# Kernel tuning notes

Hardware: AMD Instinct MI355X
Metric: run time of the kernel (lower is better)

Reference implementation:

```python
import math
import jax, jax.numpy as jnp
import numpy as np

B, T, D = 4, 2048, 1024
H, DH = 16, 64
FF = 4096
EPS = 1e-5


def setup_inputs() -> dict:
    key = jax.random.key(0)
    ks = jax.random.split(key, 12)
    s = 0.02
    inp = {
        "x": jax.random.normal(ks[0], (B, T, D), dtype=jnp.float32),
        "ln1_g": jnp.ones((D,), jnp.float32),
        "ln1_b": jnp.zeros((D,), jnp.float32),
        "ln2_g": jnp.ones((D,), jnp.float32),
        "ln2_b": jnp.zeros((D,), jnp.float32),
        # torch nn.Linear convention: weight shape [out, in], y = x @ W.T + b
        "wq": jax.random.normal(ks[1], (D, D), jnp.float32) * s,
        "bq": jnp.zeros((D,), jnp.float32),
        "wk": jax.random.normal(ks[2], (D, D), jnp.float32) * s,
        "bk": jnp.zeros((D,), jnp.float32),
        "wv": jax.random.normal(ks[3], (D, D), jnp.float32) * s,
        "bv": jnp.zeros((D,), jnp.float32),
        "wo": jax.random.normal(ks[4], (D, D), jnp.float32) * s,
        "bo": jnp.zeros((D,), jnp.float32),
        "w1": jax.random.normal(ks[5], (FF, D), jnp.float32) * s,
        "b1": jnp.zeros((FF,), jnp.float32),
        "w2": jax.random.normal(ks[6], (D, FF), jnp.float32) * s,
        "b2": jnp.zeros((D,), jnp.float32),
    }
    return inp


def _layernorm(h, g, b):
    mu = jnp.mean(h, axis=-1, keepdims=True)
    var = jnp.mean(jnp.square(h - mu), axis=-1, keepdims=True)
    return (h - mu) * jax.lax.rsqrt(var + EPS) * g + b


def _block(x, ln1_g, ln1_b, ln2_g, ln2_b, wq, bq, wk, bk, wv, bv, wo, bo, w1, b1, w2, b2):
    b, t, d = x.shape
    h = _layernorm(x, ln1_g, ln1_b)
    q = (h @ wq.T + bq).reshape(b, t, H, DH)
    k = (h @ wk.T + bk).reshape(b, t, H, DH)
    v = (h @ wv.T + bv).reshape(b, t, H, DH)
    # full (non-causal) attention, as in the torch module
    att = jnp.einsum("bqhd,bkhd->bhqk", q, k) / math.sqrt(DH)
    att = jax.nn.softmax(att, axis=-1)
    out = jnp.einsum("bhqk,bkhd->bqhd", att, v).reshape(b, t, d)
    x = x + (out @ wo.T + bo)
    h2 = _layernorm(x, ln2_g, ln2_b)
    ff = jax.nn.gelu(h2 @ w1.T + b1, approximate=False) @ w2.T + b2
    return x + ff


def reference(x, ln1_g, ln1_b, ln2_g, ln2_b, wq, bq, wk, bk, wv, bv, wo, bo, w1, b1, w2, b2):
    return _block(x, ln1_g, ln1_b, ln2_g, ln2_b, wq, bq, wk, bk, wv, bv, wo, bo, w1, b1, w2, b2)
```

## Files before the change

kernel.cpp:

```cpp
#include <hip/hip_runtime.h>
#include <cstdint>
#include <cstddef>

typedef __attribute__((ext_vector_type(8))) __bf16 bf16x8;
typedef __attribute__((ext_vector_type(4))) float f32x4;
typedef __attribute__((ext_vector_type(8))) unsigned short us8;
typedef __attribute__((ext_vector_type(4))) unsigned short us4;

__device__ inline unsigned short f2bf(float f) {
    unsigned int u = __float_as_uint(f);
    u += 0x7fffu + ((u >> 16) & 1u);
    return (unsigned short)(u >> 16);
}

__device__ inline unsigned int pkbf_t(float hi, float lo) {
    return __builtin_amdgcn_perm(__float_as_uint(hi), __float_as_uint(lo), 0x07060302u);
}

__device__ inline void async_copy16(const void* g, void* l) {
    __builtin_amdgcn_global_load_lds(
        (const __attribute__((address_space(1))) unsigned int*)g,
        (__attribute__((address_space(3))) unsigned int*)l, 16, 0, 0);
}

__global__ __launch_bounds__(256) void cvt_bf16(const float* __restrict__ in,
                                                unsigned short* __restrict__ out, int n4) {
    int i = blockIdx.x * 256 + threadIdx.x;
    if (i < n4) {
        float4 v = ((const float4*)in)[i];
        us4 o;
        o[0] = f2bf(v.x); o[1] = f2bf(v.y); o[2] = f2bf(v.z); o[3] = f2bf(v.w);
        ((us4*)out)[i] = o;
    }
}

__global__ __launch_bounds__(256) void ln_bf16(const float* __restrict__ X,
                                               const float* __restrict__ g,
                                               const float* __restrict__ b,
                                               unsigned short* __restrict__ out) {
    int row = blockIdx.x;
    int t = threadIdx.x;
    float4 v = ((const float4*)(X + (size_t)row * 1024))[t];
    float s  = v.x + v.y + v.z + v.w;
    float s2 = v.x * v.x + v.y * v.y + v.z * v.z + v.w * v.w;
#pragma unroll
    for (int m = 1; m < 64; m <<= 1) {
        s  += __shfl_xor(s, m, 64);
        s2 += __shfl_xor(s2, m, 64);
    }
    __shared__ float red[8];
    int w = t >> 6, l = t & 63;
    if (l == 0) { red[w] = s; red[4 + w] = s2; }
    __syncthreads();
    s  = red[0] + red[1] + red[2] + red[3];
    s2 = red[4] + red[5] + red[6] + red[7];
    float mu  = s * (1.0f / 1024.0f);
    float var = s2 * (1.0f / 1024.0f) - mu * mu;
    float rs  = rsqrtf(var + 1e-5f);
    int c = t * 4;
    float4 gv = *(const float4*)(g + c);
    float4 bv = *(const float4*)(b + c);
    us4 o;
    o[0] = f2bf((v.x - mu) * rs * gv.x + bv.x);
    o[1] = f2bf((v.y - mu) * rs * gv.y + bv.y);
    o[2] = f2bf((v.z - mu) * rs * gv.z + bv.z);
    o[3] = f2bf((v.w - mu) * rs * gv.w + bv.w);
    *(us4*)(out + (size_t)row * 1024 + c) = o;
}

#define BM 256
#define BN 256
#define BK 64

template <int EPI>
__global__ __launch_bounds__(512, 2) void gemm_nt(const unsigned short* __restrict__ A,
                                                  const unsigned short* __restrict__ B,
                                                  const float* __restrict__ bias,
                                                  const float* __restrict__ resid,
                                                  void* __restrict__ Cout, int N, int K) {
    __shared__ __align__(16) unsigned short As[2][BM * BK];
    __shared__ __align__(16) unsigned short Bs[2][BN * BK];
    const int tid = threadIdx.x;
    const int lane = tid & 63, w = tid >> 6;
    const int quad = lane >> 4, l16 = lane & 15;
    const int wr = w >> 2, wc = w & 3;
    const int sw = l16 & 7;

    const int gx = gridDim.x;
    const int nwg = gx * gridDim.y;
    int wg = blockIdx.y * gx + blockIdx.x;
    if (!(nwg & 7)) wg = (wg & 7) * (nwg >> 3) + (wg >> 3);
    const size_t bm = (size_t)(wg / gx) * BM;
    const size_t bn = (size_t)(wg % gx) * BN;

    const unsigned short* pA[4];
    const unsigned short* pB[4];
#pragma unroll
    for (int j = 0; j < 4; j++) {
        int c = j * 512 + tid;
        int row = c >> 3;
        int sc = (c & 7) ^ (row & 7);
        pA[j] = A + (bm + row) * (size_t)K + sc * 8;
        pB[j] = B + (bn + row) * (size_t)K + sc * 8;
    }

#define STAGE(buf, kt)                                                        \
    {                                                                         \
        const int koff = (kt)*BK;                                             \
        _Pragma("unroll") for (int j = 0; j < 4; j++)                         \
            async_copy16(pA[j] + koff, &As[buf][(j * 512 + tid) * 8]);        \
        _Pragma("unroll") for (int j = 0; j < 4; j++)                         \
            async_copy16(pB[j] + koff, &Bs[buf][(j * 512 + tid) * 8]);        \
    }

    f32x4 acc[8][4];
#pragma unroll
    for (int i = 0; i < 8; i++)
#pragma unroll
        for (int j = 0; j < 4; j++) acc[i][j] = (f32x4){0.f, 0.f, 0.f, 0.f};

    const int nk = K / BK;

    STAGE(0, 0);
    STAGE(1, 1);
    asm volatile("s_waitcnt vmcnt(8)" ::: "memory");
    __builtin_amdgcn_sched_barrier(0);
    asm volatile("s_barrier" ::: "memory");

    for (int kt = 0; kt < nk; ++kt) {
        const int r = kt & 1;
        const unsigned short* Asr = As[r];
        const unsigned short* Bsr = Bs[r];
#pragma unroll
        for (int kc = 0; kc < 2; kc++) {
            bf16x8 bfr[4];
#pragma unroll
            for (int nf = 0; nf < 4; nf++) {
                int row = wc * 64 + nf * 16 + l16;
                bfr[nf] = *(const bf16x8*)&Bsr[row * 64 + (((kc * 4 + quad) ^ sw) << 3)];
            }
#pragma unroll
            for (int mh = 0; mh < 2; mh++) {
                bf16x8 af[4];
#pragma unroll
                for (int i = 0; i < 4; i++) {
                    int row = wr * 128 + (mh * 4 + i) * 16 + l16;
                    af[i] = *(const bf16x8*)&Asr[row * 64 + (((kc * 4 + quad) ^ sw) << 3)];
                }
                __builtin_amdgcn_s_setprio(1);
#pragma unroll
                for (int i = 0; i < 4; i++)
#pragma unroll
                    for (int nf = 0; nf < 4; nf++)
                        acc[mh * 4 + i][nf] = __builtin_amdgcn_mfma_f32_16x16x32_bf16(
                            af[i], bfr[nf], acc[mh * 4 + i][nf], 0, 0, 0);
                __builtin_amdgcn_s_setprio(0);
                asm volatile("s_barrier" ::: "memory");
            }
        }
        if (kt + 2 < nk) {
            STAGE(r, kt + 2);
            asm volatile("s_waitcnt vmcnt(8)" ::: "memory");
            __builtin_amdgcn_sched_barrier(0);
            asm volatile("s_barrier" ::: "memory");
        } else if (kt + 1 < nk) {
            asm volatile("s_waitcnt vmcnt(0)" ::: "memory");
            __builtin_amdgcn_sched_barrier(0);
            asm volatile("s_barrier" ::: "memory");
        }
    }
#undef STAGE

#pragma unroll
    for (int mf = 0; mf < 8; mf++) {
#pragma unroll
        for (int nf = 0; nf < 4; nf++) {
#pragma unroll
            for (int rr = 0; rr < 4; rr++) {
                size_t row = bm + wr * 128 + mf * 16 + quad * 4 + rr;
                size_t col = bn + wc * 64 + nf * 16 + l16;
                float v = acc[mf][nf][rr] + bias[col];
                if (EPI == 1) {
                    v = 0.5f * v * (1.0f + erff(v * 0.70710678118654752f));
                    ((unsigned short*)Cout)[row * N + col] = f2bf(v);
                } else if (EPI == 2) {
                    ((float*)Cout)[row * N + col] = v + resid[row * N + col];
                } else if (EPI == 6) {
                    int sel = (int)(bn >> 10);
                    if (sel == 0) {
                        ((unsigned short*)Cout)[row * 1024 + col] =
                            f2bf(v * 0.18033688011112042f);
                    } else {
                        int key = (int)row & 2047;
                        int bh  = (((int)row >> 11) << 4) | (((int)col >> 6) & 15);
                        int dh  = (int)col & 63;
                        size_t addr;
                        if (sel == 1)
                            addr = 8388608 + (size_t)bh * 131072 +
                                   (size_t)(key >> 6) * 4096 + (size_t)(key & 63) * 64 +
                                   ((((dh >> 3) ^ (key & 7))) << 3) + (dh & 7);
                        else
                            addr = 16777216 + (size_t)bh * 131072 +
                                   (size_t)(key >> 6) * 4096 + (size_t)dh * 64 +
                                   (((((key >> 3) & 7) ^ (dh & 7))) << 3) + (key & 7);
                        ((unsigned short*)Cout)[addr] = f2bf(v);
                    }
                }
            }
        }
    }
}

__global__ __launch_bounds__(256) void attn_kernel(const unsigned short* __restrict__ Q,
                                                   const unsigned short* __restrict__ Kb,
                                                   const unsigned short* __restrict__ Vtb,
                                                   unsigned short* __restrict__ O) {
    const int bh   = blockIdx.x >> 4;
    const int qblk = blockIdx.x & 15;
    const int b = bh >> 4, h = bh & 15;
    const int tid = threadIdx.x, lane = tid & 63, w = tid >> 6;
    const int quad = lane >> 4, l16 = lane & 15;
    const int sw = l16 & 7;

    __shared__ __align__(16) unsigned short smem[20480];
    unsigned short* Vts = smem + 8192;
    unsigned short* Psw = smem + 12288 + w * 2048;

    const size_t qrow0 = (size_t)b * 2048 + (size_t)qblk * 128 + w * 32;
    const int hcol = h * 64;

    bf16x8 qfr[2][2];
#pragma unroll
    for (int qf = 0; qf < 2; qf++)
#pragma unroll
        for (int kp = 0; kp < 2; kp++)
            qfr[qf][kp] = *(const bf16x8*)(Q + (qrow0 + qf * 16 + l16) * 1024 +
                                           hcol + kp * 32 + quad * 8);

    const unsigned short* ksrc = Kb  + (size_t)bh * 131072;
    const unsigned short* vsrc = Vtb + (size_t)bh * 131072;

    async_copy16(ksrc + tid * 8,        smem + tid * 8);
    async_copy16(ksrc + 2048 + tid * 8, smem + 2048 + tid * 8);
    async_copy16(vsrc + tid * 8,        Vts + tid * 8);
    async_copy16(vsrc + 2048 + tid * 8, Vts + 2048 + tid * 8);

    f32x4 acc[4][2];
#pragma unroll
    for (int df = 0; df < 4; df++)
#pragma unroll
        for (int qf = 0; qf < 2; qf++) acc[df][qf] = (f32x4){0.f, 0.f, 0.f, 0.f};
    float l_[2] = {0.f, 0.f};

    for (int kt = 0; kt < 32; ++kt) {
        unsigned short* Ks = (kt & 1) ? (smem + 4096) : smem;
        if (kt < 31) {
            unsigned short* Kd = (kt & 1) ? smem : (smem + 4096);
            const unsigned short* kg = ksrc + (size_t)(kt + 1) * 4096;
            async_copy16(kg + tid * 8,        Kd + tid * 8);
            async_copy16(kg + 2048 + tid * 8, Kd + 2048 + tid * 8);
            asm volatile("s_waitcnt vmcnt(4)" ::: "memory");
        } else {
            asm volatile("s_waitcnt vmcnt(2)" ::: "memory");
        }
        asm volatile("s_barrier" ::: "memory");

        f32x4 s[4][2];
#pragma unroll
        for (int mf = 0; mf < 4; mf++)
#pragma unroll
            for (int qf = 0; qf < 2; qf++) s[mf][qf] = (f32x4){0.f, 0.f, 0.f, 0.f};
        __builtin_amdgcn_s_setprio(1);
#pragma unroll
        for (int kp = 0; kp < 2; kp++) {
#pragma unroll
            for (int mf = 0; mf < 4; mf++) {
                bf16x8 kf = *(const bf16x8*)&Ks[(mf * 16 + l16) * 64 +
                                                (((kp * 4 + quad) ^ sw) << 3)];
#pragma unroll
                for (int qf = 0; qf < 2; qf++)
                    s[mf][qf] = __builtin_amdgcn_mfma_f32_16x16x32_bf16(kf, qfr[qf][kp],
                                                                        s[mf][qf], 0, 0, 0);
            }
        }
        __builtin_amdgcn_s_setprio(0);

#pragma unroll
        for (int mf = 0; mf < 4; mf++)
#pragma unroll
            for (int qf = 0; qf < 2; qf++) {
                float e0 = exp2f(s[mf][qf][0]);
                float e1 = exp2f(s[mf][qf][1]);
                float e2 = exp2f(s[mf][qf][2]);
                float e3 = exp2f(s[mf][qf][3]);
                l_[qf] += (e0 + e1) + (e2 + e3);
                *(uint2*)&Psw[(qf * 16 + l16) * 64 +
                              (((mf * 2 + (quad >> 1)) ^ sw) << 3) + ((quad & 1) << 2)] =
                    make_uint2(pkbf_t(e1, e0), pkbf_t(e3, e2));
            }
        asm volatile("s_waitcnt lgkmcnt(0)" ::: "memory");

        if (kt < 31) {
            asm volatile("s_waitcnt vmcnt(2)" ::: "memory");
        } else {
            asm volatile("s_waitcnt vmcnt(0)" ::: "memory");
        }
        asm volatile("s_barrier" ::: "memory");

        __builtin_amdgcn_s_setprio(1);
#pragma unroll
        for (int kp = 0; kp < 2; kp++) {
            bf16x8 pf[2];
#pragma unroll
            for (int qf = 0; qf < 2; qf++)
                pf[qf] = *(const bf16x8*)&Psw[(qf * 16 + l16) * 64 +
                                              (((kp * 4 + quad) ^ sw) << 3)];
#pragma unroll
            for (int df = 0; df < 4; df++) {
                bf16x8 vf = *(const bf16x8*)&Vts[(df * 16 + l16) * 64 +
                                                 (((kp * 4 + quad) ^ sw) << 3)];
#pragma unroll
                for (int qf = 0; qf < 2; qf++)
                    acc[df][qf] = __builtin_amdgcn_mfma_f32_16x16x32_bf16(vf, pf[qf],
                                                                          acc[df][qf], 0, 0, 0);
            }
        }
        __builtin_amdgcn_s_setprio(0);

        asm volatile("s_barrier" ::: "memory");
        if (kt < 31) {
            const unsigned short* vg = vsrc + (size_t)(kt + 1) * 4096;
            async_copy16(vg + tid * 8,        Vts + tid * 8);
            async_copy16(vg + 2048 + tid * 8, Vts + 2048 + tid * 8);
        }
    }

#pragma unroll
    for (int qf = 0; qf < 2; qf++) {
        l_[qf] += __shfl_xor(l_[qf], 16, 64);
        l_[qf] += __shfl_xor(l_[qf], 32, 64);
    }

    __syncthreads();
    float inv[2] = {1.f / l_[0], 1.f / l_[1]};
    unsigned short* Ls = smem;
#pragma unroll
    for (int df = 0; df < 4; df++)
#pragma unroll
        for (int qf = 0; qf < 2; qf++)
#pragma unroll
            for (int r = 0; r < 4; r++) {
                int dh = df * 16 + quad * 4 + r;
                int q  = w * 32 + qf * 16 + l16;
                Ls[dh * 130 + q] =
                    (unsigned short)((__float_as_uint(acc[df][qf][r] * inv[qf]) + 0x8000u) >> 16);
            }
    __syncthreads();
    int q = tid >> 1, dh0 = (tid & 1) * 32;
    size_t obase = ((size_t)b * 2048 + (size_t)qblk * 128 + q) * 1024 + hcol + dh0;
#pragma unroll
    for (int c = 0; c < 4; c++) {
        us8 o;
#pragma unroll
        for (int j = 0; j < 8; j++) o[j] = Ls[(dh0 + c * 8 + j) * 130 + q];
        *(us8*)(O + obase + c * 8) = o;
    }
}

extern "C" void kernel_launch(void* const* d_in, const int* in_sizes, int n_in,
                              void* d_out, int out_size, void* d_ws, size_t ws_size,
                              hipStream_t stream) {
    const float* x     = (const float*)d_in[0];
    const float* ln1_g = (const float*)d_in[1];
    const float* ln1_b = (const float*)d_in[2];
    const float* ln2_g = (const float*)d_in[3];
    const float* ln2_b = (const float*)d_in[4];
    const float* wq = (const float*)d_in[5];
    const float* bq = (const float*)d_in[6];
    const float* wk = (const float*)d_in[7];
    const float* bk = (const float*)d_in[8];
    const float* wv = (const float*)d_in[9];
    const float* bv = (const float*)d_in[10];
    const float* wo = (const float*)d_in[11];
    const float* bo = (const float*)d_in[12];
    const float* w1 = (const float*)d_in[13];
    const float* b1 = (const float*)d_in[14];
    const float* w2 = (const float*)d_in[15];
    const float* b2 = (const float*)d_in[16];

    const size_t MB = 1u << 20;
    char* ws = (char*)d_ws;
    unsigned short* wqkvb = (unsigned short*)(ws + 0 * MB);
    unsigned short* wob  = (unsigned short*)(ws + 6 * MB);
    unsigned short* w1b  = (unsigned short*)(ws + 8 * MB);
    unsigned short* w2b  = (unsigned short*)(ws + 16 * MB);
    unsigned short* hb   = (unsigned short*)(ws + 24 * MB);
    unsigned short* qkvb = (unsigned short*)(ws + 40 * MB);
    unsigned short* qb   = qkvb;
    unsigned short* kblk = qkvb + 8388608;
    unsigned short* vtblk= qkvb + 16777216;
    float*          x1   = (float*)(ws + 56 * MB);
    unsigned short* h2b  = (unsigned short*)(ws + 40 * MB);
    unsigned short* ff1b = (unsigned short*)(ws + 88 * MB);
    float*          bqkv = (float*)(ws + 151 * MB);

    const int D = 1024, FF = 4096, Mrows = 8192;

    cvt_bf16<<<(D * D / 4 + 255) / 256, 256, 0, stream>>>(wq, wqkvb,               D * D / 4);
    cvt_bf16<<<(D * D / 4 + 255) / 256, 256, 0, stream>>>(wk, wqkvb + D * D,       D * D / 4);
    cvt_bf16<<<(D * D / 4 + 255) / 256, 256, 0, stream>>>(wv, wqkvb + 2 * D * D,   D * D / 4);
    cvt_bf16<<<(D * D / 4 + 255) / 256, 256, 0, stream>>>(wo, wob, D * D / 4);
    cvt_bf16<<<(FF * D / 4 + 255) / 256, 256, 0, stream>>>(w1, w1b, FF * D / 4);
    cvt_bf16<<<(FF * D / 4 + 255) / 256, 256, 0, stream>>>(w2, w2b, FF * D / 4);

    hipMemcpyAsync(bqkv,            bq, D * sizeof(float), hipMemcpyDeviceToDevice, stream);
    hipMemcpyAsync(bqkv + D,        bk, D * sizeof(float), hipMemcpyDeviceToDevice, stream);
    hipMemcpyAsync(bqkv + 2 * D,    bv, D * sizeof(float), hipMemcpyDeviceToDevice, stream);

    ln_bf16<<<Mrows, 256, 0, stream>>>(x, ln1_g, ln1_b, hb);

    dim3 gQKV(3 * D / BN, Mrows / BM);
    gemm_nt<6><<<gQKV, 512, 0, stream>>>(hb, wqkvb, bqkv, nullptr, qkvb, D, D);

    attn_kernel<<<1024, 256, 0, stream>>>(qb, kblk, vtblk, hb);

    dim3 gD(D / BN, Mrows / BM);
    gemm_nt<2><<<gD, 512, 0, stream>>>(hb, wob, bo, x, x1, D, D);

    ln_bf16<<<Mrows, 256, 0, stream>>>(x1, ln2_g, ln2_b, h2b);

    dim3 gFF(FF / BN, Mrows / BM);
    gemm_nt<1><<<gFF, 512, 0, stream>>>(h2b, w1b, b1, nullptr, ff1b, FF, D);

    gemm_nt<2><<<gD, 512, 0, stream>>>(ff1b, w2b, b2, x1, (float*)d_out, D, FF);
}
```

Before: 671.9 us.

## Template GEMM on N-tile width and use 128-wide tiles for D-output GEMMs

Makes the GEMM N-tile width a template parameter and launches the two N=1024 GEMMs (output projection and FF2) with 256x128 tiles. This doubles their workgroup count from 128 to 256 so all CUs get work. The barrier placement in the K loop is also reorganised: one barrier before the MFMA block with an explicit lgkmcnt wait, then barriers around the stage refill. Attention block indexing is remapped so that consecutive blocks cover different heads rather than the same head. The narrower tiles lower arithmetic intensity per block, and the new barrier pattern changes how loads overlap with compute.

New measurement: 630.0 us. 1.07x faster.

```diff
diff --git a/kernel.cpp b/kernel.cpp
--- a/kernel.cpp
+++ b/kernel.cpp
@@ -68,18 +68,20 @@
     *(us4*)(out + (size_t)row * 1024 + c) = o;
 }
 
-#define BM 256
-#define BN 256
-#define BK 64
-
-template <int EPI>
+template <int EPI, int BNt>
 __global__ __launch_bounds__(512, 2) void gemm_nt(const unsigned short* __restrict__ A,
                                                   const unsigned short* __restrict__ B,
                                                   const float* __restrict__ bias,
                                                   const float* __restrict__ resid,
                                                   void* __restrict__ Cout, int N, int K) {
-    __shared__ __align__(16) unsigned short As[2][BM * BK];
-    __shared__ __align__(16) unsigned short Bs[2][BN * BK];
+    constexpr int NF = BNt / 64;
+    constexpr int MH = (BNt == 256) ? 2 : 1;
+    constexpr int MF = 8 / MH;
+    constexpr int NB = BNt / 64;
+    constexpr int WTN = BNt / 4;
+
+    __shared__ __align__(16) unsigned short As[2][256 * 64];
+    __shared__ __align__(16) unsigned short Bs[2][BNt * 64];
     const int tid = threadIdx.x;
     const int lane = tid & 63, w = tid >> 6;
     const int quad = lane >> 4, l16 = lane & 15;
@@ -90,8 +92,8 @@
     const int nwg = gx * gridDim.y;
     int wg = blockIdx.y * gx + blockIdx.x;
     if (!(nwg & 7)) wg = (wg & 7) * (nwg >> 3) + (wg >> 3);
-    const size_t bm = (size_t)(wg / gx) * BM;
-    const size_t bn = (size_t)(wg % gx) * BN;
+    const size_t bm = (size_t)(wg / gx) * 256;
+    const size_t bn = (size_t)(wg % gx) * BNt;
 
     const unsigned short* pA[4];
     const unsigned short* pB[4];
@@ -101,84 +103,95 @@
         int row = c >> 3;
         int sc = (c & 7) ^ (row & 7);
         pA[j] = A + (bm + row) * (size_t)K + sc * 8;
+    }
+#pragma unroll
+    for (int j = 0; j < NB; j++) {
+        int c = j * 512 + tid;
+        int row = c >> 3;
+        int sc = (c & 7) ^ (row & 7);
         pB[j] = B + (bn + row) * (size_t)K + sc * 8;
     }
 
 #define STAGE(buf, kt)                                                        \
     {                                                                         \
-        const int koff = (kt)*BK;                                             \
+        const int koff = (kt)*64;                                             \
         _Pragma("unroll") for (int j = 0; j < 4; j++)                         \
             async_copy16(pA[j] + koff, &As[buf][(j * 512 + tid) * 8]);        \
-        _Pragma("unroll") for (int j = 0; j < 4; j++)                         \
+        _Pragma("unroll") for (int j = 0; j < NB; j++)                        \
             async_copy16(pB[j] + koff, &Bs[buf][(j * 512 + tid) * 8]);        \
     }
-
-    f32x4 acc[8][4];
+#define WAIT_LOADS()                                                          \
+    {                                                                         \
+        if constexpr (NB == 4) asm volatile("s_waitcnt vmcnt(8)" ::: "memory"); \
+        else                   asm volatile("s_waitcnt vmcnt(6)" ::: "memory"); \
+    }
+
+    f32x4 acc[8][NF];
 #pragma unroll
     for (int i = 0; i < 8; i++)
 #pragma unroll
-        for (int j = 0; j < 4; j++) acc[i][j] = (f32x4){0.f, 0.f, 0.f, 0.f};
-
-    const int nk = K / BK;
+        for (int j = 0; j < NF; j++) acc[i][j] = (f32x4){0.f, 0.f, 0.f, 0.f};
+
+    const int nk = K / 64;
 
     STAGE(0, 0);
     STAGE(1, 1);
-    asm volatile("s_waitcnt vmcnt(8)" ::: "memory");
-    __builtin_amdgcn_sched_barrier(0);
+    WAIT_LOADS();
     asm volatile("s_barrier" ::: "memory");
 
     for (int kt = 0; kt < nk; ++kt) {
-        const int r = kt & 1;
-        const unsigned short* Asr = As[r];
-        const unsigned short* Bsr = Bs[r];
+        const int cur = kt & 1;
+        const unsigned short* Asr = As[cur];
+        const unsigned short* Bsr = Bs[cur];
 #pragma unroll
         for (int kc = 0; kc < 2; kc++) {
-            bf16x8 bfr[4];
-#pragma unroll
-            for (int nf = 0; nf < 4; nf++) {
-                int row = wc * 64 + nf * 16 + l16;
+            bf16x8 bfr[NF];
+#pragma unroll
+            for (int nf = 0; nf < NF; nf++) {
+                int row = wc * WTN + nf * 16 + l16;
                 bfr[nf] = *(const bf16x8*)&Bsr[row * 64 + (((kc * 4 + quad) ^ sw) << 3)];
             }
 #pragma unroll
-            for (int mh = 0; mh < 2; mh++) {
-                bf16x8 af[4];
-#pragma unroll
-                for (int i = 0; i < 4; i++) {
-                    int row = wr * 128 + (mh * 4 + i) * 16 + l16;
+            for (int mh = 0; mh < MH; mh++) {
+                bf16x8 af[MF];
+#pragma unroll
+                for (int i = 0; i < MF; i++) {
+                    int row = wr * 128 + (mh * MF + i) * 16 + l16;
                     af[i] = *(const bf16x8*)&Asr[row * 64 + (((kc * 4 + quad) ^ sw) << 3)];
                 }
+                asm volatile("s_barrier" ::: "memory");
+                asm volatile("s_waitcnt lgkmcnt(0)" ::: "memory");
+                __builtin_amdgcn_sched_barrier(0);
                 __builtin_amdgcn_s_setprio(1);
 #pragma unroll
-                for (int i = 0; i < 4; i++)
-#pragma unroll
-                    for (int nf = 0; nf < 4; nf++)
-                        acc[mh * 4 + i][nf] = __builtin_amdgcn_mfma_f32_16x16x32_bf16(
-                            af[i], bfr[nf], acc[mh * 4 + i][nf], 0, 0, 0);
+                for (int i = 0; i < MF; i++)
+#pragma unroll
+                    for (int nf = 0; nf < NF; nf++)
+                        acc[mh * MF + i][nf] = __builtin_amdgcn_mfma_f32_16x16x32_bf16(
+                            af[i], bfr[nf], acc[mh * MF + i][nf], 0, 0, 0);
                 __builtin_amdgcn_s_setprio(0);
-                asm volatile("s_barrier" ::: "memory");
-            }
-        }
+            }
+        }
+        asm volatile("s_barrier" ::: "memory");
         if (kt + 2 < nk) {
-            STAGE(r, kt + 2);
-            asm volatile("s_waitcnt vmcnt(8)" ::: "memory");
-            __builtin_amdgcn_sched_barrier(0);
-            asm volatile("s_barrier" ::: "memory");
+            STAGE(cur, kt + 2);
+            WAIT_LOADS();
         } else if (kt + 1 < nk) {
             asm volatile("s_waitcnt vmcnt(0)" ::: "memory");
-            __builtin_amdgcn_sched_barrier(0);
-            asm volatile("s_barrier" ::: "memory");
-        }
+        }
+        asm volatile("s_barrier" ::: "memory");
     }
 #undef STAGE
+#undef WAIT_LOADS
 
 #pragma unroll
     for (int mf = 0; mf < 8; mf++) {
 #pragma unroll
-        for (int nf = 0; nf < 4; nf++) {
+        for (int nf = 0; nf < NF; nf++) {
 #pragma unroll
             for (int rr = 0; rr < 4; rr++) {
                 size_t row = bm + wr * 128 + mf * 16 + quad * 4 + rr;
-                size_t col = bn + wc * 64 + nf * 16 + l16;
+                size_t col = bn + wc * WTN + nf * 16 + l16;
                 float v = acc[mf][nf][rr] + bias[col];
                 if (EPI == 1) {
                     v = 0.5f * v * (1.0f + erff(v * 0.70710678118654752f));
@@ -215,8 +228,8 @@
                                                    const unsigned short* __restrict__ Kb,
                                                    const unsigned short* __restrict__ Vtb,
                                                    unsigned short* __restrict__ O) {
-    const int bh   = blockIdx.x >> 4;
-    const int qblk = blockIdx.x & 15;
+    const int bh   = blockIdx.x & 63;
+    const int qblk = blockIdx.x >> 6;
     const int b = bh >> 4, h = bh & 15;
     const int tid = threadIdx.x, lane = tid & 63, w = tid >> 6;
     const int quad = lane >> 4, l16 = lane & 15;
@@ -419,18 +432,18 @@
 
     ln_bf16<<<Mrows, 256, 0, stream>>>(x, ln1_g, ln1_b, hb);
 
-    dim3 gQKV(3 * D / BN, Mrows / BM);
-    gemm_nt<6><<<gQKV, 512, 0, stream>>>(hb, wqkvb, bqkv, nullptr, qkvb, D, D);
+    dim3 gQKV(3 * D / 256, Mrows / 256);
+    gemm_nt<6, 256><<<gQKV, 512, 0, stream>>>(hb, wqkvb, bqkv, nullptr, qkvb, D, D);
 
     attn_kernel<<<1024, 256, 0, stream>>>(qb, kblk, vtblk, hb);
 
-    dim3 gD(D / BN, Mrows / BM);
-    gemm_nt<2><<<gD, 512, 0, stream>>>(hb, wob, bo, x, x1, D, D);
+    dim3 gD(D / 128, Mrows / 256);
+    gemm_nt<2, 128><<<gD, 512, 0, stream>>>(hb, wob, bo, x, x1, D, D);
 
     ln_bf16<<<Mrows, 256, 0, stream>>>(x1, ln2_g, ln2_b, h2b);
 
-    dim3 gFF(FF / BN, Mrows / BM);
-    gemm_nt<1><<<gFF, 512, 0, stream>>>(h2b, w1b, b1, nullptr, ff1b, FF, D);
-
-    gemm_nt<2><<<gD, 512, 0, stream>>>(ff1b, w2b, b2, x1, (float*)d_out, D, FF);
-}
+    dim3 gFF(FF / 256, Mrows / 256);
+    gemm_nt<1, 256><<<gFF, 512, 0, stream>>>(h2b, w1b, b1, nullptr, ff1b, FF, D);
+
+    gemm_nt<2, 128><<<gD, 512, 0, stream>>>(ff1b, w2b, b2, x1, (float*)d_out, D, FF);
+}
```
